# Performance work log

Measured on AMD Instinct MI355X. Metric: run time of the kernel, lower is better.

The kernel has to match this reference:

```python
import jax, jax.numpy as jnp
import numpy as np

B, H, W, C = 8, 64, 64, 256
C8 = C // 8  # query/key channels


def setup_inputs() -> dict:
    key = jax.random.key(0)
    ks = jax.random.split(key, 8)
    s = 0.02  # init scale for weights
    return {
        "x": jax.random.normal(ks[0], (B, H, W, C), dtype=jnp.float32),
        "Wq": jax.random.normal(ks[1], (C, C8), dtype=jnp.float32) * s,
        "bq": jnp.zeros((C8,), dtype=jnp.float32),
        "Wk": jax.random.normal(ks[2], (C, C8), dtype=jnp.float32) * s,
        "bk": jnp.zeros((C8,), dtype=jnp.float32),
        "Wv": jax.random.normal(ks[3], (C, C), dtype=jnp.float32) * s,
        "bv": jnp.zeros((C,), dtype=jnp.float32),
        "gamma": jnp.full((1,), 0.5, dtype=jnp.float32),
    }


def reference(x, Wq, bq, Wk, bk, Wv, bv, gamma):
    Bn, Hn, Wn, Cn = x.shape
    N = Hn * Wn
    xf = x.reshape(Bn, N, Cn)            # flatten spatial dims: [B, N, C]
    # 1x1 convs == per-pixel dense projections over channels
    q = xf @ Wq + bq                     # [B, N, C//8]
    k = xf @ Wk + bk                     # [B, N, C//8]
    v = xf @ Wv + bv                     # [B, N, C]
    # energy[b,i,j] = k_i . q_j  (matches tf.matmul(key, query, transpose_b=True))
    energy = jnp.einsum('bic,bjc->bij', k, q)   # [B, N, N]
    attn = jax.nn.softmax(energy, axis=-1)      # softmax over last axis
    # out_i = sum_j attn[i,j] * v_j  (intended SAGAN aggregation in NHWC layout)
    out = jnp.einsum('bij,bjc->bic', attn, v)   # [B, N, C]
    out = out.reshape(Bn, Hn, Wn, Cn)
    return gamma * out + x
```

## Files before the change

### kernel.cpp

```cpp
#include <hip/hip_runtime.h>

typedef __attribute__((ext_vector_type(8))) short short8;
typedef __attribute__((ext_vector_type(4))) float f32x4;
typedef __attribute__((ext_vector_type(16))) float f32x16;
typedef __attribute__((ext_vector_type(2))) unsigned int u32x2;
typedef __attribute__((ext_vector_type(4))) unsigned int u32x4;
typedef unsigned short u16;
typedef unsigned int u32;

#define MFMA16(a, b, c) __builtin_amdgcn_mfma_f32_16x16x32_bf16((a), (b), (c), 0, 0, 0)
#define MFMA32(a, b, c) __builtin_amdgcn_mfma_f32_32x32x16_bf16((a), (b), (c), 0, 0, 0)

#define BAR_VMEM() asm volatile("s_waitcnt vmcnt(0) lgkmcnt(0)\ns_barrier" ::: "memory")
#define BAR_LDS()  asm volatile("s_waitcnt lgkmcnt(0)\ns_barrier" ::: "memory")

#define BATCH 8
#define NTOK 4096
#define CDIM 256
#define CQK 32
#define LOG2E 1.4426950408889634f

__device__ __forceinline__ u16 f2bf(float f) {
  u32 u = __float_as_uint(f);
  return (u16)((u + 0x7FFFu + ((u >> 16) & 1u)) >> 16);
}
__device__ __forceinline__ u32 pack2(float a, float b) {
  const u32 ua = __float_as_uint(a) + 0x8000u;
  const u32 ub = __float_as_uint(b) + 0x8000u;
#if __has_builtin(__builtin_amdgcn_perm)
  return __builtin_amdgcn_perm(ub, ua, 0x07060302u);
#else
  return (ua >> 16) | (ub & 0xFFFF0000u);
#endif
}
__device__ __forceinline__ float fexp2(float x) {
#if __has_builtin(__builtin_amdgcn_exp2f)
  return __builtin_amdgcn_exp2f(x);
#else
  return exp2f(x);
#endif
}

__global__ void k_prep(const float* __restrict__ Wq, const float* __restrict__ bq,
                       const float* __restrict__ Wk, const float* __restrict__ bk,
                       const float* __restrict__ Wv, const float* __restrict__ bv,
                       u16* __restrict__ wtf, float* __restrict__ bias) {
  const int f = blockIdx.x;
  const int L = threadIdx.x;
  const int ct = f >> 3, ks = f & 7;
  const int o = ct * 16 + (L & 15);
  const int ch = ks * 32 + (L >> 4) * 8;
  short8 v8;
#pragma unroll
  for (int jj = 0; jj < 8; jj++) {
    const int c = ch + jj;
    float v;
    if (o < 32)       v = Wq[c * CQK + o];
    else if (o < 64)  v = Wk[c * CQK + (o - 32)];
    else              v = Wv[c * CDIM + (o - 64)];
    v8[jj] = (short)f2bf(v);
  }
  *(short8*)(wtf + (size_t)f * 512 + L * 8) = v8;
  if (f == 0) {
    for (int i = L; i < 320; i += 64) {
      if (i < 32)      bias[i] = bq[i];
      else if (i < 64) bias[i] = bk[i - 32];
      else             bias[i] = bv[i - 64];
    }
  }
}

__global__ __launch_bounds__(256, 2) void k_proj(
    const float* __restrict__ x, const u16* __restrict__ wtf,
    const float* __restrict__ bias,
    u16* __restrict__ q_ws, u16* __restrict__ k_ws, u16* __restrict__ vt_ws) {
  __shared__ u16 x_lds[64 * 264];
  __shared__ u16 vt_t[64 * 72];
  const int m0 = blockIdx.x * 64;
  const int tid = threadIdx.x;
  const int w = tid >> 6, L = tid & 63;
  const int lr = L & 15, q4 = L >> 4;

  short8 wfA[5], wfB[5];
#pragma unroll
  for (int j = 0; j < 5; j++)
    wfA[j] = *(const short8*)(wtf + ((size_t)((j * 4 + w) * 8 + 0)) * 512 + L * 8);

#pragma unroll
  for (int ii = 0; ii < 8; ii++) {
    const int e = (tid + 256 * ii) * 8;
    const int row = e >> 8, col = e & 255;
    const float* src = x + (size_t)(m0 + row) * CDIM + col;
    f32x4 a = *(const f32x4*)src;
    f32x4 b4 = *(const f32x4*)(src + 4);
    u32x4 pk;
    pk[0] = pack2(a[0], a[1]);
    pk[1] = pack2(a[2], a[3]);
    pk[2] = pack2(b4[0], b4[1]);
    pk[3] = pack2(b4[2], b4[3]);
    *(u32x4*)&x_lds[row * 264 + col] = pk;
  }
  __syncthreads();

  f32x4 acc[4][5];
#pragma unroll
  for (int rg = 0; rg < 4; rg++)
#pragma unroll
    for (int j = 0; j < 5; j++) acc[rg][j] = (f32x4){0.f, 0.f, 0.f, 0.f};

#pragma unroll
  for (int ks = 0; ks < 8; ks++) {
    if (ks < 7) {
#pragma unroll
      for (int j = 0; j < 5; j++) {
        short8 v = *(const short8*)(wtf +
            ((size_t)((j * 4 + w) * 8 + ks + 1)) * 512 + L * 8);
        if (ks & 1) wfA[j] = v; else wfB[j] = v;
      }
    }
#pragma unroll
    for (int rg = 0; rg < 4; rg++) {
      short8 a = *(const short8*)&x_lds[(rg * 16 + lr) * 264 + ks * 32 + q4 * 8];
#pragma unroll
      for (int j = 0; j < 5; j++)
        acc[rg][j] = MFMA16(a, (ks & 1) ? wfB[j] : wfA[j], acc[rg][j]);
    }
  }

  {
    const float bb = bias[w * 16 + lr];
#pragma unroll
    for (int rg = 0; rg < 4; rg++)
#pragma unroll
      for (int r = 0; r < 4; r++) {
        const int row = m0 + rg * 16 + q4 * 4 + r;
        float v = acc[rg][0][r] + bb;
        if (w < 2) q_ws[(size_t)row * CQK + w * 16 + lr] = f2bf(v);
        else       k_ws[(size_t)row * CQK + (w - 2) * 16 + lr] = f2bf(v * LOG2E);
      }
  }
  const int b = m0 >> 12, nt = (m0 & 4095) >> 6;
  const int rb2 = ((lr >> 3) & 1) << 2;
  const int c_l = w * 16 + lr;
#pragma unroll
  for (int cg = 0; cg < 4; cg++) {
    __syncthreads();
    const int j = cg + 1;
    const float bb = bias[(4 + cg * 4 + w) * 16 + lr];
#pragma unroll
    for (int rg = 0; rg < 4; rg++) {
      const int n_base = (rg * 16 + q4 * 4) ^ rb2;
      u32x2 pk;
      pk[0] = pack2(acc[rg][j][0] + bb, acc[rg][j][1] + bb);
      pk[1] = pack2(acc[rg][j][2] + bb, acc[rg][j][3] + bb);
      *(u32x2*)&vt_t[c_l * 72 + n_base] = pk;
    }
    __syncthreads();
#pragma unroll
    for (int i = 0; i < 2; i++) {
      const int gch = tid + 256 * i;
      const int fi = gch >> 6;
      const int lane = gch & 63;
      const int ks2 = fi >> 1, ct2 = fi & 1;
      short8 v = *(const short8*)&vt_t[(ct2 * 32 + (lane & 31)) * 72 +
                                       (ks2 * 2 + (lane >> 5)) * 8];
      *(short8*)(vt_ws +
          ((((size_t)(b * 64 + nt) * 4 + cg) * 8 + fi) * 512) + lane * 8) = v;
    }
  }
}

__global__ __launch_bounds__(256, 2) void k_attn(
    const float* __restrict__ x, const u16* __restrict__ q_ws,
    const u16* __restrict__ k_ws, const u16* __restrict__ vt_ws,
    const float* __restrict__ gamma, float* __restrict__ out) {
  __shared__ u16 p_lds[2][64 * 64];

  const int bid = blockIdx.x;
  const int b = bid & 7;
  const int it = bid >> 3;
  const int i0 = it * 64;
  const int tid = threadIdx.x;
  const int w = tid >> 6, L = tid & 63;
  const int lr = L & 15, q4 = L >> 4;
  const int L31 = L & 31, Lhi = L >> 5, L7 = L & 7;

  const short8 a_k = *(const short8*)(k_ws +
      ((size_t)(b * NTOK + i0 + w * 16 + lr)) * CQK + q4 * 8);

  const u16* vg = vt_ws + (((size_t)b * 256 + w) * 8) * 512 + (size_t)L * 8;
  const u16* q_base = q_ws + (size_t)b * NTOK * CQK;

  f32x16 o_acc[2][2];
#pragma unroll
  for (int ih = 0; ih < 2; ih++)
#pragma unroll
    for (int ct2 = 0; ct2 < 2; ct2++)
#pragma unroll
      for (int e = 0; e < 16; e++) o_acc[ih][ct2][e] = 0.f;
  float lsum = 0.f;

  const int pw_off = (w * 16 + lr) * 64 + (((q4 & 1) ^ ((lr >> 3) & 1)) << 2);
  const int q4h = q4 >> 1;
  u16* const pl0 = &p_lds[0][0];
  u16* const pl1 = &p_lds[1][0];

#define EXPW(SV, T, PW)                                                          \
  do {                                                                           \
    const float p0 = fexp2((SV)[0]);                                             \
    const float p1 = fexp2((SV)[1]);                                             \
    const float p2 = fexp2((SV)[2]);                                             \
    const float p3 = fexp2((SV)[3]);                                             \
    lsum += (p0 + p1) + (p2 + p3);                                               \
    u32x2 pk;                                                                    \
    pk[0] = pack2(p0, p1);                                                       \
    pk[1] = pack2(p2, p3);                                                       \
    *(u32x2*)((PW) + (((2 * (T) + q4h) ^ (lr & 7)) * 8)) = pk;                   \
  } while (0)

  short8 bqA[4], bqB[4];
  short8 vV[8];
#pragma unroll
  for (int t = 0; t < 4; t++)
    bqA[t] = *(const short8*)(q_base + (size_t)(t * 16 + lr) * CQK + q4 * 8);
#pragma unroll
  for (int fi = 0; fi < 8; fi++)
    vV[fi] = *(const short8*)(vg + (size_t)fi * 512);
  {
    f32x4 s0 = MFMA16(bqA[0], a_k, ((f32x4){0.f, 0.f, 0.f, 0.f}));
    f32x4 s1 = MFMA16(bqA[1], a_k, ((f32x4){0.f, 0.f, 0.f, 0.f}));
    f32x4 s2 = MFMA16(bqA[2], a_k, ((f32x4){0.f, 0.f, 0.f, 0.f}));
    f32x4 s3 = MFMA16(bqA[3], a_k, ((f32x4){0.f, 0.f, 0.f, 0.f}));
    u16* pwn = pl0 + pw_off;
    EXPW(s0, 0, pwn);
    EXPW(s1, 1, pwn);
    EXPW(s2, 2, pwn);
    EXPW(s3, 3, pwn);
  }
#pragma unroll
  for (int t = 0; t < 4; t++)
    bqB[t] = *(const short8*)(q_base + (size_t)(64 + t * 16 + lr) * CQK + q4 * 8);

#define ATTN_ITER(JT, PL_CUR, PL_NXT, BQN, BQF, DO_Q)                            \
  do {                                                                           \
    BAR_LDS();          \
    f32x4 s0 = MFMA16(BQN[0], a_k, ((f32x4){0.f, 0.f, 0.f, 0.f}));               \
    f32x4 s1 = MFMA16(BQN[1], a_k, ((f32x4){0.f, 0.f, 0.f, 0.f}));               \
    f32x4 s2 = MFMA16(BQN[2], a_k, ((f32x4){0.f, 0.f, 0.f, 0.f}));               \
    f32x4 s3 = MFMA16(BQN[3], a_k, ((f32x4){0.f, 0.f, 0.f, 0.f}));               \
    if (DO_Q) {                                                                  \
      _Pragma("unroll")                                                          \
      for (int t = 0; t < 4; t++)                                                \
        BQF[t] = *(const short8*)(q_base +                                       \
                 (size_t)((JT) * 64 + 128 + t * 16 + lr) * CQK + q4 * 8);        \
    }                                                                            \
    u16* pwn = (PL_NXT) + pw_off;                                                \
    _Pragma("unroll")                                                            \
    for (int ks = 0; ks < 4; ks++) {                                             \
      const int slot = (((ks * 2 + Lhi) ^ L7)) * 8;                              \
      short8 a_p0 = *(const short8*)((PL_CUR) + L31 * 64 + slot);                \
      short8 a_p1 = *(const short8*)((PL_CUR) + (32 + L31) * 64 + slot);         \
      o_acc[0][0] = MFMA32(a_p0, vV[ks * 2 + 0], o_acc[0][0]);                   \
      o_acc[1][0] = MFMA32(a_p1, vV[ks * 2 + 0], o_acc[1][0]);                   \
      o_acc[0][1] = MFMA32(a_p0, vV[ks * 2 + 1], o_acc[0][1]);                   \
      o_acc[1][1] = MFMA32(a_p1, vV[ks * 2 + 1], o_acc[1][1]);                   \
      vV[ks * 2 + 0] = *(const short8*)(vg +                                     \
          (size_t)((JT) + 1) * 16384 + (ks * 2 + 0) * 512);                      \
      vV[ks * 2 + 1] = *(const short8*)(vg +                                     \
          (size_t)((JT) + 1) * 16384 + (ks * 2 + 1) * 512);                      \
      if (ks == 0) EXPW(s0, 0, pwn);                                             \
      if (ks == 1) EXPW(s1, 1, pwn);                                             \
      if (ks == 2) EXPW(s2, 2, pwn);                                             \
      if (ks == 3) EXPW(s3, 3, pwn);                                             \
    }                                                                            \
  } while (0)

  for (int jt2 = 0; jt2 < 62; jt2 += 2) {
    ATTN_ITER(jt2,     pl0, pl1, bqB, bqA, 1);
    ATTN_ITER(jt2 + 1, pl1, pl0, bqA, bqB, 1);
  }
  ATTN_ITER(62, pl0, pl1, bqB, bqA, 0);
#undef ATTN_ITER

  BAR_LDS();
#pragma unroll
  for (int ks = 0; ks < 4; ks++) {
    const int slot = (((ks * 2 + Lhi) ^ L7)) * 8;
    short8 a_p0 = *(const short8*)(pl1 + L31 * 64 + slot);
    short8 a_p1 = *(const short8*)(pl1 + (32 + L31) * 64 + slot);
    o_acc[0][0] = MFMA32(a_p0, vV[ks * 2 + 0], o_acc[0][0]);
    o_acc[1][0] = MFMA32(a_p1, vV[ks * 2 + 0], o_acc[1][0]);
    o_acc[0][1] = MFMA32(a_p0, vV[ks * 2 + 1], o_acc[0][1]);
    o_acc[1][1] = MFMA32(a_p1, vV[ks * 2 + 1], o_acc[1][1]);
  }
#undef EXPW

  float s2 = lsum;
  s2 += __shfl_xor(s2, 16);
  s2 += __shfl_xor(s2, 32);
  const float rl = 1.0f / s2;
  BAR_LDS();
  float* lp = (float*)pl0;
  if (q4 == 0) lp[w * 16 + lr] = rl;
  BAR_LDS();

  float linv2[2][16];
#pragma unroll
  for (int ih = 0; ih < 2; ih++)
#pragma unroll
    for (int rg = 0; rg < 16; rg++)
      linv2[ih][rg] = lp[ih * 32 + (rg & 3) + 8 * (rg >> 2) + 4 * Lhi];

  const float g = gamma[0];
#pragma unroll
  for (int ih = 0; ih < 2; ih++)
#pragma unroll
    for (int ct2 = 0; ct2 < 2; ct2++) {
      const int c = w * 64 + ct2 * 32 + L31;
#pragma unroll
      for (int rg = 0; rg < 16; rg++) {
        const int i = i0 + ih * 32 + (rg & 3) + 8 * (rg >> 2) + 4 * Lhi;
        const size_t idx = ((size_t)(b * NTOK + i)) * CDIM + c;
        out[idx] = g * (o_acc[ih][ct2][rg] * linv2[ih][rg]) + x[idx];
      }
    }
}

extern "C" void kernel_launch(void* const* d_in, const int* in_sizes, int n_in,
                              void* d_out, int out_size, void* d_ws, size_t ws_size,
                              hipStream_t stream) {
  const float* x  = (const float*)d_in[0];
  const float* Wq = (const float*)d_in[1];
  const float* bq = (const float*)d_in[2];
  const float* Wk = (const float*)d_in[3];
  const float* bk = (const float*)d_in[4];
  const float* Wv = (const float*)d_in[5];
  const float* bv = (const float*)d_in[6];
  const float* gamma = (const float*)d_in[7];
  float* out = (float*)d_out;

  char* ws = (char*)d_ws;
  u16* q_ws  = (u16*)(ws);
  u16* k_ws  = (u16*)(ws + (2u << 20));
  u16* vt_ws = (u16*)(ws + (4u << 20));
  u16* wtf   = (u16*)(ws + (20u << 20));
  float* bias = (float*)(ws + (20u << 20) + (256u << 10));

  k_prep<<<160, 64, 0, stream>>>(Wq, bq, Wk, bk, Wv, bv, wtf, bias);
  k_proj<<<512, 256, 0, stream>>>(x, wtf, bias, q_ws, k_ws, vt_ws);
  k_attn<<<512, 256, 0, stream>>>(x, q_ws, k_ws, vt_ws, gamma, out);
}
```

Before: 185.1 us.

## Split attention work across eight waves per block instead of four

Doubles the k_attn block to 512 threads. Each wave now computes half of the QK score tiles (split by jh) and owns 32 output channels instead of 64. The row sums from the two wave halves are combined through LDS with extra barriers before normalisation. The aim is to cut per-wave register pressure and raise latency hiding through more waves per CU, at the cost of extra barrier synchronisation and duplicated P-tile LDS reads.

```diff
diff --git a/kernel.cpp b/kernel.cpp
--- a/kernel.cpp
+++ b/kernel.cpp
@@ -170,7 +170,7 @@
   }
 }
 
-__global__ __launch_bounds__(256, 2) void k_attn(
+__global__ __launch_bounds__(512, 4) void k_attn(
     const float* __restrict__ x, const u16* __restrict__ q_ws,
     const u16* __restrict__ k_ws, const u16* __restrict__ vt_ws,
     const float* __restrict__ gamma, float* __restrict__ out) {
@@ -184,23 +184,24 @@
   const int w = tid >> 6, L = tid & 63;
   const int lr = L & 15, q4 = L >> 4;
   const int L31 = L & 31, Lhi = L >> 5, L7 = L & 7;
+  const int isub = w & 3;
+  const int jh = w >> 2;
 
   const short8 a_k = *(const short8*)(k_ws +
-      ((size_t)(b * NTOK + i0 + w * 16 + lr)) * CQK + q4 * 8);
-
-  const u16* vg = vt_ws + (((size_t)b * 256 + w) * 8) * 512 + (size_t)L * 8;
+      ((size_t)(b * NTOK + i0 + isub * 16 + lr)) * CQK + q4 * 8);
+
+  const u16* vg = vt_ws +
+      ((((size_t)b * 64) * 4 + (w >> 1)) * 8 + (w & 1)) * 512 + (size_t)L * 8;
   const u16* q_base = q_ws + (size_t)b * NTOK * CQK;
 
-  f32x16 o_acc[2][2];
+  f32x16 o_acc[2];
 #pragma unroll
   for (int ih = 0; ih < 2; ih++)
 #pragma unroll
-    for (int ct2 = 0; ct2 < 2; ct2++)
-#pragma unroll
-      for (int e = 0; e < 16; e++) o_acc[ih][ct2][e] = 0.f;
+    for (int e = 0; e < 16; e++) o_acc[ih][e] = 0.f;
   float lsum = 0.f;
 
-  const int pw_off = (w * 16 + lr) * 64 + (((q4 & 1) ^ ((lr >> 3) & 1)) << 2);
+  const int pw_off = (isub * 16 + lr) * 64 + (((q4 & 1) ^ ((lr >> 3) & 1)) << 2);
   const int q4h = q4 >> 1;
   u16* const pl0 = &p_lds[0][0];
   u16* const pl1 = &p_lds[1][0];
@@ -218,41 +219,37 @@
     *(u32x2*)((PW) + (((2 * (T) + q4h) ^ (lr & 7)) * 8)) = pk;                   \
   } while (0)
 
-  short8 bqA[4], bqB[4];
-  short8 vV[8];
-#pragma unroll
-  for (int t = 0; t < 4; t++)
-    bqA[t] = *(const short8*)(q_base + (size_t)(t * 16 + lr) * CQK + q4 * 8);
-#pragma unroll
-  for (int fi = 0; fi < 8; fi++)
-    vV[fi] = *(const short8*)(vg + (size_t)fi * 512);
+  short8 bqA[2], bqB[2];
+  short8 vV[4];
+#pragma unroll
+  for (int tt = 0; tt < 2; tt++)
+    bqA[tt] = *(const short8*)(q_base +
+        (size_t)((jh * 2 + tt) * 16 + lr) * CQK + q4 * 8);
+#pragma unroll
+  for (int ks = 0; ks < 4; ks++)
+    vV[ks] = *(const short8*)(vg + (size_t)ks * 1024);
   {
     f32x4 s0 = MFMA16(bqA[0], a_k, ((f32x4){0.f, 0.f, 0.f, 0.f}));
     f32x4 s1 = MFMA16(bqA[1], a_k, ((f32x4){0.f, 0.f, 0.f, 0.f}));
-    f32x4 s2 = MFMA16(bqA[2], a_k, ((f32x4){0.f, 0.f, 0.f, 0.f}));
-    f32x4 s3 = MFMA16(bqA[3], a_k, ((f32x4){0.f, 0.f, 0.f, 0.f}));
     u16* pwn = pl0 + pw_off;
-    EXPW(s0, 0, pwn);
-    EXPW(s1, 1, pwn);
-    EXPW(s2, 2, pwn);
-    EXPW(s3, 3, pwn);
-  }
-#pragma unroll
-  for (int t = 0; t < 4; t++)
-    bqB[t] = *(const short8*)(q_base + (size_t)(64 + t * 16 + lr) * CQK + q4 * 8);
+    EXPW(s0, jh * 2 + 0, pwn);
+    EXPW(s1, jh * 2 + 1, pwn);
+  }
+#pragma unroll
+  for (int tt = 0; tt < 2; tt++)
+    bqB[tt] = *(const short8*)(q_base +
+        (size_t)(64 + (jh * 2 + tt) * 16 + lr) * CQK + q4 * 8);
 
 #define ATTN_ITER(JT, PL_CUR, PL_NXT, BQN, BQF, DO_Q)                            \
   do {                                                                           \
     BAR_LDS();          \
     f32x4 s0 = MFMA16(BQN[0], a_k, ((f32x4){0.f, 0.f, 0.f, 0.f}));               \
     f32x4 s1 = MFMA16(BQN[1], a_k, ((f32x4){0.f, 0.f, 0.f, 0.f}));               \
-    f32x4 s2 = MFMA16(BQN[2], a_k, ((f32x4){0.f, 0.f, 0.f, 0.f}));               \
-    f32x4 s3 = MFMA16(BQN[3], a_k, ((f32x4){0.f, 0.f, 0.f, 0.f}));               \
     if (DO_Q) {                                                                  \
       _Pragma("unroll")                                                          \
-      for (int t = 0; t < 4; t++)                                                \
-        BQF[t] = *(const short8*)(q_base +                                       \
-                 (size_t)((JT) * 64 + 128 + t * 16 + lr) * CQK + q4 * 8);        \
+      for (int tt = 0; tt < 2; tt++)                                             \
+        BQF[tt] = *(const short8*)(q_base +                                      \
+            (size_t)((JT) * 64 + 128 + (jh * 2 + tt) * 16 + lr) * CQK + q4 * 8); \
     }                                                                            \
     u16* pwn = (PL_NXT) + pw_off;                                                \
     _Pragma("unroll")                                                            \
@@ -260,18 +257,12 @@
       const int slot = (((ks * 2 + Lhi) ^ L7)) * 8;                              \
       short8 a_p0 = *(const short8*)((PL_CUR) + L31 * 64 + slot);                \
       short8 a_p1 = *(const short8*)((PL_CUR) + (32 + L31) * 64 + slot);         \
-      o_acc[0][0] = MFMA32(a_p0, vV[ks * 2 + 0], o_acc[0][0]);                   \
-      o_acc[1][0] = MFMA32(a_p1, vV[ks * 2 + 0], o_acc[1][0]);                   \
-      o_acc[0][1] = MFMA32(a_p0, vV[ks * 2 + 1], o_acc[0][1]);                   \
-      o_acc[1][1] = MFMA32(a_p1, vV[ks * 2 + 1], o_acc[1][1]);                   \
-      vV[ks * 2 + 0] = *(const short8*)(vg +                                     \
-          (size_t)((JT) + 1) * 16384 + (ks * 2 + 0) * 512);                      \
-      vV[ks * 2 + 1] = *(const short8*)(vg +                                     \
-          (size_t)((JT) + 1) * 16384 + (ks * 2 + 1) * 512);                      \
-      if (ks == 0) EXPW(s0, 0, pwn);                                             \
-      if (ks == 1) EXPW(s1, 1, pwn);                                             \
-      if (ks == 2) EXPW(s2, 2, pwn);                                             \
-      if (ks == 3) EXPW(s3, 3, pwn);                                             \
+      o_acc[0] = MFMA32(a_p0, vV[ks], o_acc[0]);                                 \
+      o_acc[1] = MFMA32(a_p1, vV[ks], o_acc[1]);                                 \
+      vV[ks] = *(const short8*)(vg +                                             \
+          (size_t)((JT) + 1) * 16384 + ks * 1024);                               \
+      if (ks == 0) EXPW(s0, jh * 2 + 0, pwn);                                    \
+      if (ks == 2) EXPW(s1, jh * 2 + 1, pwn);                                    \
     }                                                                            \
   } while (0)
 
@@ -288,20 +279,21 @@
     const int slot = (((ks * 2 + Lhi) ^ L7)) * 8;
     short8 a_p0 = *(const short8*)(pl1 + L31 * 64 + slot);
     short8 a_p1 = *(const short8*)(pl1 + (32 + L31) * 64 + slot);
-    o_acc[0][0] = MFMA32(a_p0, vV[ks * 2 + 0], o_acc[0][0]);
-    o_acc[1][0] = MFMA32(a_p1, vV[ks * 2 + 0], o_acc[1][0]);
-    o_acc[0][1] = MFMA32(a_p0, vV[ks * 2 + 1], o_acc[0][1]);
-    o_acc[1][1] = MFMA32(a_p1, vV[ks * 2 + 1], o_acc[1][1]);
+    o_acc[0] = MFMA32(a_p0, vV[ks], o_acc[0]);
+    o_acc[1] = MFMA32(a_p1, vV[ks], o_acc[1]);
   }
 #undef EXPW
 
   float s2 = lsum;
   s2 += __shfl_xor(s2, 16);
   s2 += __shfl_xor(s2, 32);
-  const float rl = 1.0f / s2;
   BAR_LDS();
   float* lp = (float*)pl0;
-  if (q4 == 0) lp[w * 16 + lr] = rl;
+  if (jh == 0 && q4 == 0) lp[isub * 16 + lr] = s2;
+  BAR_LDS();
+  if (jh == 1 && q4 == 0) lp[isub * 16 + lr] += s2;
+  BAR_LDS();
+  if (jh == 0 && q4 == 0) lp[isub * 16 + lr] = 1.0f / lp[isub * 16 + lr];
   BAR_LDS();
 
   float linv2[2][16];
@@ -312,17 +304,14 @@
       linv2[ih][rg] = lp[ih * 32 + (rg & 3) + 8 * (rg >> 2) + 4 * Lhi];
 
   const float g = gamma[0];
+  const int c = w * 32 + L31;
 #pragma unroll
   for (int ih = 0; ih < 2; ih++)
 #pragma unroll
-    for (int ct2 = 0; ct2 < 2; ct2++) {
-      const int c = w * 64 + ct2 * 32 + L31;
-#pragma unroll
-      for (int rg = 0; rg < 16; rg++) {
-        const int i = i0 + ih * 32 + (rg & 3) + 8 * (rg >> 2) + 4 * Lhi;
-        const size_t idx = ((size_t)(b * NTOK + i)) * CDIM + c;
-        out[idx] = g * (o_acc[ih][ct2][rg] * linv2[ih][rg]) + x[idx];
-      }
+    for (int rg = 0; rg < 16; rg++) {
+      const int i = i0 + ih * 32 + (rg & 3) + 8 * (rg >> 2) + 4 * Lhi;
+      const size_t idx = ((size_t)(b * NTOK + i)) * CDIM + c;
+      out[idx] = g * (o_acc[ih][rg] * linv2[ih][rg]) + x[idx];
     }
 }
 
@@ -348,5 +337,5 @@
 
   k_prep<<<160, 64, 0, stream>>>(Wq, bq, Wk, bk, Wv, bv, wtf, bias);
   k_proj<<<512, 256, 0, stream>>>(x, wtf, bias, q_ws, k_ws, vt_ws);
-  k_attn<<<512, 256, 0, stream>>>(x, q_ws, k_ws, vt_ws, gamma, out);
-}
+  k_attn<<<512, 512, 0, stream>>>(x, q_ws, k_ws, vt_ws, gamma, out);
+}
```

Result: no change. 187.0 us (+1.0%).

## Enlarge attention row tile to 128 with 8 waves per block

Applied to the files above, without the earlier changes.

Doubles the query-row tile per block from 64 to 128 and uses 512 threads (8 waves), halving the grid. Each wave now owns a 32-channel slice of V across all 128 rows, so each V fragment loaded feeds four MFMAs instead of two, which roughly halves the V traffic per output. The trade-offs are twice the LDS for the P buffers, a larger block, and a different column split across waves. Fewer blocks (256) may also leave some CUs underfilled.

```diff
diff --git a/kernel.cpp b/kernel.cpp
--- a/kernel.cpp
+++ b/kernel.cpp
@@ -170,16 +170,16 @@
   }
 }
 
-__global__ __launch_bounds__(256, 2) void k_attn(
+__global__ __launch_bounds__(512, 2) void k_attn(
     const float* __restrict__ x, const u16* __restrict__ q_ws,
     const u16* __restrict__ k_ws, const u16* __restrict__ vt_ws,
     const float* __restrict__ gamma, float* __restrict__ out) {
-  __shared__ u16 p_lds[2][64 * 64];
+  __shared__ u16 p_lds[2][128 * 64];
 
   const int bid = blockIdx.x;
   const int b = bid & 7;
   const int it = bid >> 3;
-  const int i0 = it * 64;
+  const int i0 = it * 128;
   const int tid = threadIdx.x;
   const int w = tid >> 6, L = tid & 63;
   const int lr = L & 15, q4 = L >> 4;
@@ -188,16 +188,15 @@
   const short8 a_k = *(const short8*)(k_ws +
       ((size_t)(b * NTOK + i0 + w * 16 + lr)) * CQK + q4 * 8);
 
-  const u16* vg = vt_ws + (((size_t)b * 256 + w) * 8) * 512 + (size_t)L * 8;
+  const u16* vg = vt_ws +
+      ((size_t)b * 2048 + (w >> 1) * 8 + (w & 1)) * 512 + (size_t)L * 8;
   const u16* q_base = q_ws + (size_t)b * NTOK * CQK;
 
-  f32x16 o_acc[2][2];
-#pragma unroll
-  for (int ih = 0; ih < 2; ih++)
-#pragma unroll
-    for (int ct2 = 0; ct2 < 2; ct2++)
-#pragma unroll
-      for (int e = 0; e < 16; e++) o_acc[ih][ct2][e] = 0.f;
+  f32x16 o_acc[4];
+#pragma unroll
+  for (int ig = 0; ig < 4; ig++)
+#pragma unroll
+    for (int e = 0; e < 16; e++) o_acc[ig][e] = 0.f;
   float lsum = 0.f;
 
   const int pw_off = (w * 16 + lr) * 64 + (((q4 & 1) ^ ((lr >> 3) & 1)) << 2);
@@ -219,13 +218,13 @@
   } while (0)
 
   short8 bqA[4], bqB[4];
-  short8 vV[8];
+  short8 vV[4];
 #pragma unroll
   for (int t = 0; t < 4; t++)
     bqA[t] = *(const short8*)(q_base + (size_t)(t * 16 + lr) * CQK + q4 * 8);
 #pragma unroll
-  for (int fi = 0; fi < 8; fi++)
-    vV[fi] = *(const short8*)(vg + (size_t)fi * 512);
+  for (int ks2 = 0; ks2 < 4; ks2++)
+    vV[ks2] = *(const short8*)(vg + (size_t)ks2 * 1024);
   {
     f32x4 s0 = MFMA16(bqA[0], a_k, ((f32x4){0.f, 0.f, 0.f, 0.f}));
     f32x4 s1 = MFMA16(bqA[1], a_k, ((f32x4){0.f, 0.f, 0.f, 0.f}));
@@ -256,22 +255,22 @@
     }                                                                            \
     u16* pwn = (PL_NXT) + pw_off;                                                \
     _Pragma("unroll")                                                            \
-    for (int ks = 0; ks < 4; ks++) {                                             \
-      const int slot = (((ks * 2 + Lhi) ^ L7)) * 8;                              \
-      short8 a_p0 = *(const short8*)((PL_CUR) + L31 * 64 + slot);                \
+    for (int ks2 = 0; ks2 < 4; ks2++) {                                          \
+      const int slot = (((ks2 * 2 + Lhi) ^ L7)) * 8;                             \
+      short8 a_p0 = *(const short8*)((PL_CUR) + (L31) * 64 + slot);              \
       short8 a_p1 = *(const short8*)((PL_CUR) + (32 + L31) * 64 + slot);         \
-      o_acc[0][0] = MFMA32(a_p0, vV[ks * 2 + 0], o_acc[0][0]);                   \
-      o_acc[1][0] = MFMA32(a_p1, vV[ks * 2 + 0], o_acc[1][0]);                   \
-      o_acc[0][1] = MFMA32(a_p0, vV[ks * 2 + 1], o_acc[0][1]);                   \
-      o_acc[1][1] = MFMA32(a_p1, vV[ks * 2 + 1], o_acc[1][1]);                   \
-      vV[ks * 2 + 0] = *(const short8*)(vg +                                     \
-          (size_t)((JT) + 1) * 16384 + (ks * 2 + 0) * 512);                      \
-      vV[ks * 2 + 1] = *(const short8*)(vg +                                     \
-          (size_t)((JT) + 1) * 16384 + (ks * 2 + 1) * 512);                      \
-      if (ks == 0) EXPW(s0, 0, pwn);                                             \
-      if (ks == 1) EXPW(s1, 1, pwn);                                             \
-      if (ks == 2) EXPW(s2, 2, pwn);                                             \
-      if (ks == 3) EXPW(s3, 3, pwn);                                             \
+      short8 a_p2 = *(const short8*)((PL_CUR) + (64 + L31) * 64 + slot);         \
+      short8 a_p3 = *(const short8*)((PL_CUR) + (96 + L31) * 64 + slot);         \
+      o_acc[0] = MFMA32(a_p0, vV[ks2], o_acc[0]);                                \
+      o_acc[1] = MFMA32(a_p1, vV[ks2], o_acc[1]);                                \
+      o_acc[2] = MFMA32(a_p2, vV[ks2], o_acc[2]);                                \
+      o_acc[3] = MFMA32(a_p3, vV[ks2], o_acc[3]);                                \
+      vV[ks2] = *(const short8*)(vg +                                            \
+          (size_t)((JT) + 1) * 16384 + ks2 * 1024);                              \
+      if (ks2 == 0) EXPW(s0, 0, pwn);                                            \
+      if (ks2 == 1) EXPW(s1, 1, pwn);                                            \
+      if (ks2 == 2) EXPW(s2, 2, pwn);                                            \
+      if (ks2 == 3) EXPW(s3, 3, pwn);                                            \
     }                                                                            \
   } while (0)
 
@@ -284,14 +283,16 @@
 
   BAR_LDS();
 #pragma unroll
-  for (int ks = 0; ks < 4; ks++) {
-    const int slot = (((ks * 2 + Lhi) ^ L7)) * 8;
-    short8 a_p0 = *(const short8*)(pl1 + L31 * 64 + slot);
+  for (int ks2 = 0; ks2 < 4; ks2++) {
+    const int slot = (((ks2 * 2 + Lhi) ^ L7)) * 8;
+    short8 a_p0 = *(const short8*)(pl1 + (L31) * 64 + slot);
     short8 a_p1 = *(const short8*)(pl1 + (32 + L31) * 64 + slot);
-    o_acc[0][0] = MFMA32(a_p0, vV[ks * 2 + 0], o_acc[0][0]);
-    o_acc[1][0] = MFMA32(a_p1, vV[ks * 2 + 0], o_acc[1][0]);
-    o_acc[0][1] = MFMA32(a_p0, vV[ks * 2 + 1], o_acc[0][1]);
-    o_acc[1][1] = MFMA32(a_p1, vV[ks * 2 + 1], o_acc[1][1]);
+    short8 a_p2 = *(const short8*)(pl1 + (64 + L31) * 64 + slot);
+    short8 a_p3 = *(const short8*)(pl1 + (96 + L31) * 64 + slot);
+    o_acc[0] = MFMA32(a_p0, vV[ks2], o_acc[0]);
+    o_acc[1] = MFMA32(a_p1, vV[ks2], o_acc[1]);
+    o_acc[2] = MFMA32(a_p2, vV[ks2], o_acc[2]);
+    o_acc[3] = MFMA32(a_p3, vV[ks2], o_acc[3]);
   }
 #undef EXPW
 
@@ -304,25 +305,22 @@
   if (q4 == 0) lp[w * 16 + lr] = rl;
   BAR_LDS();
 
-  float linv2[2][16];
-#pragma unroll
-  for (int ih = 0; ih < 2; ih++)
+  float linv[4][16];
+#pragma unroll
+  for (int ig = 0; ig < 4; ig++)
 #pragma unroll
     for (int rg = 0; rg < 16; rg++)
-      linv2[ih][rg] = lp[ih * 32 + (rg & 3) + 8 * (rg >> 2) + 4 * Lhi];
+      linv[ig][rg] = lp[ig * 32 + (rg & 3) + 8 * (rg >> 2) + 4 * Lhi];
 
   const float g = gamma[0];
-#pragma unroll
-  for (int ih = 0; ih < 2; ih++)
-#pragma unroll
-    for (int ct2 = 0; ct2 < 2; ct2++) {
-      const int c = w * 64 + ct2 * 32 + L31;
-#pragma unroll
-      for (int rg = 0; rg < 16; rg++) {
-        const int i = i0 + ih * 32 + (rg & 3) + 8 * (rg >> 2) + 4 * Lhi;
-        const size_t idx = ((size_t)(b * NTOK + i)) * CDIM + c;
-        out[idx] = g * (o_acc[ih][ct2][rg] * linv2[ih][rg]) + x[idx];
-      }
+  const int c = (w >> 1) * 64 + (w & 1) * 32 + L31;
+#pragma unroll
+  for (int ig = 0; ig < 4; ig++)
+#pragma unroll
+    for (int rg = 0; rg < 16; rg++) {
+      const int i = i0 + ig * 32 + (rg & 3) + 8 * (rg >> 2) + 4 * Lhi;
+      const size_t idx = ((size_t)(b * NTOK + i)) * CDIM + c;
+      out[idx] = g * (o_acc[ig][rg] * linv[ig][rg]) + x[idx];
     }
 }
 
@@ -348,5 +346,5 @@
 
   k_prep<<<160, 64, 0, stream>>>(Wq, bq, Wk, bk, Wv, bv, wtf, bias);
   k_proj<<<512, 256, 0, stream>>>(x, wtf, bias, q_ws, k_ws, vt_ws);
-  k_attn<<<512, 256, 0, stream>>>(x, q_ws, k_ws, vt_ws, gamma, out);
-}
+  k_attn<<<256, 512, 0, stream>>>(x, q_ws, k_ws, vt_ws, gamma, out);
+}
```

Measured after the change: 185.4 us. No clear change (+0.2%).
